# Kernel optimization log

Measured on AMD Instinct MI355X. Metric: run time of the kernel, lower is better.

Reference implementation:

```python
import jax, jax.numpy as jnp
import numpy as np

B, S, D, H, L = 2, 2048, 768, 12, 12
DH = D // H
REL_POS_BINS, MAX_REL_POS = 32, 128
REL_2D_POS_BINS, MAX_REL_2D_POS = 64, 256
LN_EPS = 1e-12


def setup_inputs() -> dict:
    key = jax.random.key(0)
    ks = jax.random.split(key, 12)
    s = 0.02
    return {
        "hidden_states": jax.random.normal(ks[0], (B, S, D), jnp.float32),
        "attention_mask": jnp.zeros((B, 1, 1, S), jnp.bool_),  # True = masked
        "position_ids": jnp.sort(jax.random.randint(ks[1], (B, S), 0, 1024), axis=-1),
        "bbox": jax.random.randint(ks[2], (B, S, 4), 0, 1024),
        # stacked per-layer params (torch Linear applied as x @ W + b)
        "q_w": jax.random.normal(ks[3], (L, D, D), jnp.float32) * s,
        "q_b": jnp.zeros((L, D), jnp.float32),
        "k_w": jax.random.normal(ks[4], (L, D, D), jnp.float32) * s,
        "k_b": jnp.zeros((L, D), jnp.float32),
        "v_w": jax.random.normal(ks[5], (L, D, D), jnp.float32) * s,
        "v_b": jnp.zeros((L, D), jnp.float32),
        "o_w": jax.random.normal(ks[6], (L, D, D), jnp.float32) * s,
        "o_b": jnp.zeros((L, D), jnp.float32),
        "ln_g": jnp.ones((L, D), jnp.float32),
        "ln_b": jnp.zeros((L, D), jnp.float32),
        # rel-pos bias heads x buckets (nn.Linear(bins, heads, bias=False).weight)
        "rel_pos_bias_w": jax.random.normal(ks[7], (H, REL_POS_BINS), jnp.float32) * s,
        "rel_x_bias_w": jax.random.normal(ks[8], (H, REL_2D_POS_BINS), jnp.float32) * s,
        "rel_y_bias_w": jax.random.normal(ks[9], (H, REL_2D_POS_BINS), jnp.float32) * s,
    }


def _rel_bucket(rel, num_buckets, max_distance):
    # bidirectional bucketing from Mesh-TF / ErnieLayout
    nb = num_buckets // 2
    ret = (rel > 0).astype(jnp.int32) * nb
    n = jnp.abs(rel).astype(jnp.int32)
    max_exact = nb // 2
    is_small = n < max_exact
    nf = jnp.maximum(n, 1).astype(jnp.float32)  # avoid log(0); masked by is_small
    val_large = max_exact + (
        jnp.log(nf / max_exact) / np.log(max_distance / max_exact) * (nb - max_exact)
    ).astype(jnp.int32)
    val_large = jnp.minimum(val_large, nb - 1)
    return ret + jnp.where(is_small, n, val_large)


def _bias_from_table(ids_1d, table, num_buckets, max_distance):
    # ids_1d: [B,S] int; table: [H, buckets] -> bias [B,H,S,S]
    rel = ids_1d[:, None, :] - ids_1d[:, :, None]  # memory - query
    buckets = _rel_bucket(rel, num_buckets, max_distance)  # [B,S,S]
    return jnp.transpose(table.T[buckets], (0, 3, 1, 2))  # one-hot @ W.T == gather


def _layer_norm(x, g, b):
    m = jnp.mean(x, axis=-1, keepdims=True)
    v = jnp.mean((x - m) ** 2, axis=-1, keepdims=True)
    return (x - m) / jnp.sqrt(v + LN_EPS) * g + b


def reference(hidden_states, attention_mask, position_ids, bbox,
              q_w, q_b, k_w, k_b, v_w, v_b, o_w, o_b, ln_g, ln_b,
              rel_pos_bias_w, rel_x_bias_w, rel_y_bias_w):
    rel_pos = _bias_from_table(position_ids, rel_pos_bias_w, REL_POS_BINS, MAX_REL_POS)
    rel_2d = (_bias_from_table(bbox[:, :, 0], rel_x_bias_w, REL_2D_POS_BINS, MAX_REL_2D_POS)
              + _bias_from_table(bbox[:, :, 3], rel_y_bias_w, REL_2D_POS_BINS, MAX_REL_2D_POS))
    bias = rel_pos + rel_2d  # [B,H,S,S], shared across layers
    neg = jnp.finfo(jnp.float32).min
    inv_sqrt_dh = 1.0 / np.sqrt(DH)

    def layer(h, p):
        qw, qb, kw, kb, vw, vb, ow, ob, g, bb = p
        q = (h @ qw + qb).reshape(B, S, H, DH).transpose(0, 2, 1, 3) * inv_sqrt_dh
        k = (h @ kw + kb).reshape(B, S, H, DH).transpose(0, 2, 1, 3)
        v = (h @ vw + vb).reshape(B, S, H, DH).transpose(0, 2, 1, 3)
        scores = jnp.einsum('bhqd,bhkd->bhqk', q, k) + bias
        scores = jnp.where(attention_mask, neg, scores)
        probs = jax.nn.softmax(scores, axis=-1)
        ctx = jnp.einsum('bhqk,bhkd->bhqd', probs, v).transpose(0, 2, 1, 3).reshape(B, S, D)
        out = ctx @ ow + ob  # ErnieLayoutSelfOutput dense
        return _layer_norm(out + h, g, bb), None

    h, _ = jax.lax.scan(layer, hidden_states,
                        (q_w, q_b, k_w, k_b, v_w, v_b, o_w, o_b, ln_g, ln_b))
    return h
```

## Files before the change

### kernel.cpp

```cpp
#include <hip/hip_runtime.h>


#define BB 2
#define SS 2048
#define DD 768
#define HH 12
#define NLAYER 12
#define MM 4096

typedef unsigned short u16;
typedef __attribute__((ext_vector_type(8))) short bf16x8;
typedef __attribute__((ext_vector_type(4))) float f32x4;

#define LOG2E 1.44269504088896340736f

__device__ __forceinline__ u16 f2bf(float f) {
  unsigned u = __float_as_uint(f);
  unsigned r = (u + 0x7FFFu + ((u >> 16) & 1u)) >> 16;
  return (u16)r;
}
__device__ __forceinline__ float bf2f(unsigned u) {
  return __uint_as_float(u << 16);
}
__device__ __forceinline__ unsigned cvtpk(float a, float b) {
  unsigned r;
  asm("v_cvt_pk_bf16_f32 %0, %1, %2" : "=v"(r) : "v"(a), "v"(b));
  return r;
}
__device__ __forceinline__ float exp2v(float x) {
  float r;
  asm("v_exp_f32 %0, %1" : "=v"(r) : "v"(x));
  return r;
}

__device__ __forceinline__ void g2lds16(const void* g, void* l) {
  __builtin_amdgcn_global_load_lds(
      (const __attribute__((address_space(1))) unsigned int*)g,
      (__attribute__((address_space(3))) unsigned int*)l, 16, 0, 0);
}

__global__ __launch_bounds__(256) void k_hb(const float4* __restrict__ x,
                                            uint2* __restrict__ o, int n4) {
  int i = blockIdx.x * 256 + threadIdx.x;
  if (i < n4) {
    float4 v = x[i];
    uint2 r;
    r.x = (unsigned)f2bf(v.x) | ((unsigned)f2bf(v.y) << 16);
    r.y = (unsigned)f2bf(v.z) | ((unsigned)f2bf(v.w) << 16);
    o[i] = r;
  }
}

__device__ __forceinline__ int bucket1(int rel) {
  int ret = rel > 0 ? 16 : 0;
  int n = rel < 0 ? -rel : rel;
  if (n < 8) return ret + n;
  int v = 8 + (int)(logf((float)n * 0.125f) * 2.8853900817779268f);
  return ret + (v < 15 ? v : 15);
}
__device__ __forceinline__ int bucket2(int rel) {
  int ret = rel > 0 ? 32 : 0;
  int n = rel < 0 ? -rel : rel;
  if (n < 16) return ret + n;
  int v = 16 + (int)(logf((float)n * 0.0625f) * 5.7707801635558537f);
  return ret + (v < 31 ? v : 31);
}

__global__ __launch_bounds__(256) void k_bias(
    const int* __restrict__ pos, const int* __restrict__ bbx,
    const unsigned char* __restrict__ msk,
    const float* __restrict__ wp, const float* __restrict__ wx,
    const float* __restrict__ wy, u16* __restrict__ bias) {
  int bid = blockIdx.x;
  int b = bid >> 10, qt = (bid >> 5) & 31, kt = bid & 31;
  __shared__ float swp[384], swx[768], swy[768];
  __shared__ int pq[64], xq[64], yq[64], pk[64], xk[64], yk[64];
  __shared__ unsigned char mk[64];
  int t = threadIdx.x;
  for (int i = t; i < 384; i += 256) swp[i] = wp[i];
  for (int i = t; i < 768; i += 256) { swx[i] = wx[i]; swy[i] = wy[i]; }
  int q0 = qt * 64, k0 = kt * 64;
  if (t < 64) {
    int gi = b * SS + q0 + t;
    pq[t] = pos[gi]; xq[t] = bbx[gi * 4]; yq[t] = bbx[gi * 4 + 3];
  } else if (t < 128) {
    int j = t - 64, gi = b * SS + k0 + j;
    pk[j] = pos[gi]; xk[j] = bbx[gi * 4]; yk[j] = bbx[gi * 4 + 3];
    mk[j] = msk[b * SS + k0 + j];
  }
  __syncthreads();
  int w = t >> 6, l = t & 63;
  int hi = l >> 4;
  int qlr = w * 16 + (l & 15);
  int pql = pq[qlr], xql = xq[qlr], yql = yq[qlr];
  int packed[16];
#pragma unroll
  for (int fn = 0; fn < 4; fn++)
#pragma unroll
    for (int r = 0; r < 4; r++) {
      int kl = fn * 16 + hi * 4 + r;
      int b1 = bucket1(pk[kl] - pql);
      int b2 = bucket2(xk[kl] - xql);
      int b3 = bucket2(yk[kl] - yql);
      packed[fn * 4 + r] = b1 | (b2 << 5) | (b3 << 11) | (mk[kl] ? (1 << 17) : 0);
    }
  for (int h = 0; h < 12; h++) {
    const float* rp = swp + h * 32;
    const float* rx = swx + h * 64;
    const float* ry = swy + h * 64;
    unsigned pk2[8];
#pragma unroll
    for (int j = 0; j < 8; j++) {
      int p0 = packed[2 * j], p1 = packed[2 * j + 1];
      float f0 = (rp[p0 & 31] + rx[(p0 >> 5) & 63] + ry[(p0 >> 11) & 63]) * LOG2E;
      float f1 = (rp[p1 & 31] + rx[(p1 >> 5) & 63] + ry[(p1 >> 11) & 63]) * LOG2E;
      if (p0 >> 17) f0 = -3.0e38f;
      if (p1 >> 17) f1 = -3.0e38f;
      pk2[j] = (unsigned)f2bf(f0) | ((unsigned)f2bf(f1) << 16);
    }
    u16* dst = bias +
        ((size_t)((b * 12 + h) * 1024 + qt * 32 + kt) * 256 + t) * 16;
    ((uint4*)dst)[0] = make_uint4(pk2[0], pk2[1], pk2[2], pk2[3]);
    ((uint4*)dst)[1] = make_uint4(pk2[4], pk2[5], pk2[6], pk2[7]);
  }
}

__global__ __launch_bounds__(256) void k_wconv(
    const float* __restrict__ qw, const float* __restrict__ kw,
    const float* __restrict__ vw, const float* __restrict__ ow, int layer,
    u16* __restrict__ wt) {
  int bid = blockIdx.x;
  int g = bid / 576, rr_ = bid % 576, nt = rr_ / 24, kt = rr_ % 24;
  const float* src = g == 0 ? qw : g == 1 ? kw : g == 2 ? vw : ow;
  src += (size_t)layer * DD * DD;
  __shared__ float sm[32][33];
  int t = threadIdx.x, c = t & 31, r0 = t >> 5;
#pragma unroll
  for (int p = 0; p < 4; p++) {
    int rr = r0 + p * 8;
    sm[rr][c] = src[(size_t)(kt * 32 + rr) * DD + nt * 32 + c];
  }
  __syncthreads();
  u16* dst = wt + (size_t)g * DD * DD;
#pragma unroll
  for (int p = 0; p < 4; p++) {
    int rn = r0 + p * 8;
    dst[(size_t)(nt * 32 + rn) * DD + kt * 32 + c] = f2bf(sm[c][rn]);
  }
}

__device__ __forceinline__ void gemm_core(const u16* __restrict__ A,
                                          const u16* __restrict__ Bt, u16* As,
                                          u16* Bs, f32x4 acc[4][4], int tid) {
  int w = tid >> 6, l = tid & 63;
  int wm = w >> 1, wn = w & 1;
#pragma unroll
  for (int i = 0; i < 4; i++)
#pragma unroll
    for (int j = 0; j < 4; j++) acc[i][j] = f32x4{0.f, 0.f, 0.f, 0.f};
  for (int kt = 0; kt < 12; kt++) {
    __syncthreads();
    int r0 = w * 32;
#pragma unroll
    for (int j = 0; j < 4; j++) {
      int row = r0 + j * 8 + (l >> 3);
      int sl = (l & 7) ^ (row & 7);
      g2lds16(A + (size_t)row * DD + kt * 64 + sl * 8, As + (r0 + j * 8) * 64);
      g2lds16(Bt + (size_t)row * DD + kt * 64 + sl * 8, Bs + (r0 + j * 8) * 64);
    }
    __syncthreads();
#pragma unroll
    for (int kk = 0; kk < 2; kk++) {
      bf16x8 af[4], bfr[4];
#pragma unroll
      for (int fm = 0; fm < 4; fm++) {
        int row = wm * 64 + fm * 16 + (l & 15);
        int slot = (kk * 4 + (l >> 4)) ^ (row & 7);
        af[fm] = *(const bf16x8*)((const char*)As + row * 128 + slot * 16);
      }
#pragma unroll
      for (int fn = 0; fn < 4; fn++) {
        int row = wn * 64 + fn * 16 + (l & 15);
        int slot = (kk * 4 + (l >> 4)) ^ (row & 7);
        bfr[fn] = *(const bf16x8*)((const char*)Bs + row * 128 + slot * 16);
      }
#pragma unroll
      for (int fm = 0; fm < 4; fm++)
#pragma unroll
        for (int fn = 0; fn < 4; fn++)
          acc[fm][fn] = __builtin_amdgcn_mfma_f32_16x16x32_bf16(
              af[fm], bfr[fn], acc[fm][fn], 0, 0, 0);
    }
  }
}

__global__ __launch_bounds__(256) void k_gemm_qkv(
    const u16* __restrict__ hb, const u16* __restrict__ wt,
    const float* __restrict__ qbias, const float* __restrict__ kbias,
    const float* __restrict__ vbias, u16* __restrict__ qo, u16* __restrict__ ko,
    u16* __restrict__ vo) {
  __shared__ __align__(16) u16 As[128 * 64];
  __shared__ __align__(16) u16 Bs[128 * 64];
  int bid = blockIdx.x;
  int mblk = bid / 18, nblk = bid % 18;
  int g = nblk / 6, nb = nblk % 6;
  const u16* A = hb + (size_t)mblk * 128 * DD;
  const u16* Bt = wt + (size_t)g * DD * DD + (size_t)nb * 128 * DD;
  f32x4 acc[4][4];
  gemm_core(A, Bt, As, Bs, acc, threadIdx.x);
  const float* bias = g == 0 ? qbias : g == 1 ? kbias : vbias;
  u16* out = g == 0 ? qo : g == 1 ? ko : vo;
  float scale = g == 0 ? 0.125f * LOG2E : 1.0f;
  int w = threadIdx.x >> 6, l = threadIdx.x & 63;
  int wm = w >> 1, wn = w & 1;
#pragma unroll
  for (int fn = 0; fn < 4; fn++) {
    int col = nb * 128 + wn * 64 + fn * 16 + (l & 15);
    float bval = bias[col];
#pragma unroll
    for (int fm = 0; fm < 4; fm++)
#pragma unroll
      for (int r = 0; r < 4; r++) {
        int row = mblk * 128 + wm * 64 + fm * 16 + ((l >> 4) << 2) + r;
        out[(size_t)row * DD + col] = f2bf((acc[fm][fn][r] + bval) * scale);
      }
  }
}

__global__ __launch_bounds__(256) void k_gemm_o(const u16* __restrict__ ctx,
                                                const u16* __restrict__ wto,
                                                const float* __restrict__ obias,
                                                float* __restrict__ outp) {
  __shared__ __align__(16) u16 As[128 * 64];
  __shared__ __align__(16) u16 Bs[128 * 64];
  int bid = blockIdx.x;
  int mblk = bid / 6, nblk = bid % 6;
  const u16* A = ctx + (size_t)mblk * 128 * DD;
  const u16* Bt = wto + (size_t)nblk * 128 * DD;
  f32x4 acc[4][4];
  gemm_core(A, Bt, As, Bs, acc, threadIdx.x);
  int w = threadIdx.x >> 6, l = threadIdx.x & 63;
  int wm = w >> 1, wn = w & 1;
#pragma unroll
  for (int fn = 0; fn < 4; fn++) {
    int col = nblk * 128 + wn * 64 + fn * 16 + (l & 15);
    float bval = obias[col];
#pragma unroll
    for (int fm = 0; fm < 4; fm++)
#pragma unroll
      for (int r = 0; r < 4; r++) {
        int row = mblk * 128 + wm * 64 + fm * 16 + ((l >> 4) << 2) + r;
        outp[(size_t)row * DD + col] = acc[fm][fn][r] + bval;
      }
  }
}

__global__ __launch_bounds__(256) void k_vt(const u16* __restrict__ vo,
                                            u16* __restrict__ vt) {
  int bid = blockIdx.x;
  int bh = bid >> 5, st = bid & 31;
  int b = bh / 12, h = bh % 12;
  int s0 = st * 64;
  __shared__ u16 sm[64][68];
  int t = threadIdx.x, c = t & 63, r0 = t >> 6;
#pragma unroll
  for (int p = 0; p < 16; p++) {
    int r = r0 + p * 4;
    sm[r][c] = vo[(size_t)(b * SS + s0 + r) * DD + h * 64 + c];
  }
  __syncthreads();
#pragma unroll
  for (int p = 0; p < 16; p++) {
    int d = r0 + p * 4;
    vt[(size_t)(bh * 64 + d) * SS + s0 + c] = sm[c][d];
  }
}

__global__ __launch_bounds__(256) void k_attn(
    const u16* __restrict__ qm, const u16* __restrict__ kmat,
    const u16* __restrict__ vt, const u16* __restrict__ bias,
    u16* __restrict__ ctx) {
  int bid = blockIdx.x;
  int qt = bid & 31, bh = bid >> 5;
  int b = bh / 12, h = bh % 12;
  __shared__ __align__(16) u16 Ks[2][64 * 64];
  __shared__ __align__(16) u16 Vs[2][64 * 64];
  __shared__ __align__(16) u16 Ps[4][16 * 64];
  int tid = threadIdx.x, w = tid >> 6, l = tid & 63;
  int hi = l >> 4, qr = l & 15;
  int q0 = qt * 64;
  const u16* qp = qm + (size_t)(b * SS + q0 + w * 16 + qr) * DD + h * 64 +
                  hi * 8;
  bf16x8 aq0 = *(const bf16x8*)qp;
  bf16x8 aq1 = *(const bf16x8*)(qp + 32);
  const u16* kb_ = kmat + (size_t)(b * SS) * DD + h * 64;
  const u16* vb_ = vt + (size_t)bh * 64 * SS;
  const u16* bb_ = bias + ((size_t)(bh * 32 + qt) * 32 * 256 + tid) * 16;
  f32x4 oa[4];
#pragma unroll
  for (int fn = 0; fn < 4; fn++) oa[fn] = f32x4{0.f, 0.f, 0.f, 0.f};
  float m_ = -3.0e38f, l_ = 0.f;
  int srow = tid >> 3, sc8 = tid & 7;

  auto STAGE = [&](int kt, int buf) {
#pragma unroll
    for (int j = 0; j < 2; j++) {
      int rr = srow + j * 32;
      int sl = sc8 ^ (rr & 7);
      g2lds16(kb_ + (size_t)(kt * 64 + rr) * DD + sl * 8,
              &Ks[buf][tid * 8 + j * 2048]);
      g2lds16(vb_ + (size_t)rr * SS + kt * 64 + sl * 8,
              &Vs[buf][tid * 8 + j * 2048]);
    }
  };

  STAGE(0, 0);
  uint4 bu0 = ((const uint4*)bb_)[0];
  uint4 bu1 = ((const uint4*)bb_)[1];
  uint4 nb0 = bu0, nb1 = bu1;
  char* pw = (char*)&Ps[w][0] + qr * 128;
  int qs = (qr & 7) << 4;
  __syncthreads();

  for (int kt = 0; kt < 32; kt++) {
    int buf = kt & 1;
    if (kt < 31) STAGE(kt + 1, buf ^ 1);
    f32x4 sc[4];
#pragma unroll
    for (int fn = 0; fn < 4; fn++) sc[fn] = f32x4{0.f, 0.f, 0.f, 0.f};
#pragma unroll
    for (int kk = 0; kk < 2; kk++) {
      bf16x8 aq = kk == 0 ? aq0 : aq1;
#pragma unroll
      for (int fn = 0; fn < 4; fn++) {
        int row = fn * 16 + qr;
        int slot = (kk * 4 + hi) ^ (row & 7);
        bf16x8 bk = *(const bf16x8*)((const char*)&Ks[buf][0] + row * 128 +
                                     slot * 16);
        sc[fn] = __builtin_amdgcn_mfma_f32_16x16x32_bf16(bk, aq, sc[fn],
                                                         0, 0, 0);
      }
    }
    unsigned ua[8] = {bu0.x, bu0.y, bu0.z, bu0.w, bu1.x, bu1.y, bu1.z, bu1.w};
#pragma unroll
    for (int fn = 0; fn < 4; fn++)
#pragma unroll
      for (int r = 0; r < 4; r++) {
        int i = fn * 4 + r;
        unsigned uv = ua[i >> 1];
        sc[fn][r] += bf2f((i & 1) ? (uv >> 16) : (uv & 0xffffu));
      }
    if (kt < 31) {
      const uint4* bpn = (const uint4*)(bb_ + (size_t)(kt + 1) * 4096);
      nb0 = bpn[0];
      nb1 = bpn[1];
    }
    float pm = fmaxf(fmaxf(fmaxf(sc[0][0], sc[0][1]), fmaxf(sc[0][2], sc[0][3])),
                     fmaxf(fmaxf(sc[1][0], sc[1][1]), fmaxf(sc[1][2], sc[1][3])));
    pm = fmaxf(pm,
         fmaxf(fmaxf(fmaxf(sc[2][0], sc[2][1]), fmaxf(sc[2][2], sc[2][3])),
               fmaxf(fmaxf(sc[3][0], sc[3][1]), fmaxf(sc[3][2], sc[3][3]))));
    pm = fmaxf(pm, __shfl_xor(pm, 16));
    pm = fmaxf(pm, __shfl_xor(pm, 32));
    if (__any(pm > m_)) {
      float mn = fmaxf(m_, pm);
      float f = exp2v(m_ - mn);
#pragma unroll
      for (int fn = 0; fn < 4; fn++)
#pragma unroll
        for (int r = 0; r < 4; r++) oa[fn][r] *= f;
      l_ *= f;
      m_ = mn;
    }
    float rs = 0.f;
#pragma unroll
    for (int fn = 0; fn < 4; fn++)
#pragma unroll
      for (int r = 0; r < 4; r++) {
        float pv = exp2v(sc[fn][r] - m_);
        sc[fn][r] = pv;
        rs += pv;
      }
    rs += __shfl_xor(rs, 16);
    rs += __shfl_xor(rs, 32);
    l_ += rs;
#pragma unroll
    for (int fn = 0; fn < 4; fn++) {
      unsigned w0 = cvtpk(sc[fn][0], sc[fn][1]);
      unsigned w1 = cvtpk(sc[fn][2], sc[fn][3]);
      *(uint2*)(pw + ((fn * 32 + hi * 8) ^ qs)) = make_uint2(w0, w1);
    }
#pragma unroll
    for (int ck = 0; ck < 2; ck++) {
      bf16x8 pt = *(const bf16x8*)(pw + ((ck * 64 + hi * 16) ^ qs));
#pragma unroll
      for (int fn = 0; fn < 4; fn++) {
        int row = fn * 16 + qr;
        int slot = (ck * 4 + hi) ^ (row & 7);
        bf16x8 av = *(const bf16x8*)((const char*)&Vs[buf][0] + row * 128 +
                                     slot * 16);
        oa[fn] = __builtin_amdgcn_mfma_f32_16x16x32_bf16(av, pt, oa[fn],
                                                         0, 0, 0);
      }
    }
    bu0 = nb0;
    bu1 = nb1;
    __syncthreads();
  }
  float inv = 1.0f / l_;
  u16* cp = ctx + (size_t)(b * SS + q0 + w * 16 + qr) * DD + h * 64 + hi * 4;
#pragma unroll
  for (int fn = 0; fn < 4; fn++) {
    unsigned w0 = cvtpk(oa[fn][0] * inv, oa[fn][1] * inv);
    unsigned w1 = cvtpk(oa[fn][2] * inv, oa[fn][3] * inv);
    *(uint2*)(cp + fn * 16) = make_uint2(w0, w1);
  }
}

__global__ __launch_bounds__(256) void k_ln(const float* __restrict__ x,
                                            const float* __restrict__ res,
                                            const float* __restrict__ g,
                                            const float* __restrict__ bta,
                                            float* __restrict__ ho,
                                            u16* __restrict__ hbo) {
  int row = blockIdx.x;
  int t = threadIdx.x;
  const float* xr = x + (size_t)row * DD;
  const float* rr = res + (size_t)row * DD;
  float v[3];
  float s = 0.f, s2 = 0.f;
#pragma unroll
  for (int j = 0; j < 3; j++) {
    float a = xr[t + j * 256] + rr[t + j * 256];
    v[j] = a;
    s += a;
    s2 += a * a;
  }
#pragma unroll
  for (int m = 1; m < 64; m <<= 1) {
    s += __shfl_xor(s, m);
    s2 += __shfl_xor(s2, m);
  }
  __shared__ float red[8];
  int w = t >> 6, l = t & 63;
  if (l == 0) { red[w] = s; red[4 + w] = s2; }
  __syncthreads();
  s = red[0] + red[1] + red[2] + red[3];
  s2 = red[4] + red[5] + red[6] + red[7];
  float mean = s * (1.f / 768.f);
  float var = s2 * (1.f / 768.f) - mean * mean;
  float rstd = rsqrtf(var + 1e-12f);
#pragma unroll
  for (int j = 0; j < 3; j++) {
    int c = t + j * 256;
    float y = (v[j] - mean) * rstd * g[c] + bta[c];
    ho[(size_t)row * DD + c] = y;
    hbo[(size_t)row * DD + c] = f2bf(y);
  }
}

extern "C" void kernel_launch(void* const* d_in, const int* in_sizes, int n_in,
                              void* d_out, int out_size, void* d_ws,
                              size_t ws_size, hipStream_t stream) {
  const float* hid = (const float*)d_in[0];
  const unsigned char* msk = (const unsigned char*)d_in[1];
  const int* pos = (const int*)d_in[2];
  const int* bbx = (const int*)d_in[3];
  const float* qw = (const float*)d_in[4];
  const float* qbv = (const float*)d_in[5];
  const float* kw = (const float*)d_in[6];
  const float* kbv = (const float*)d_in[7];
  const float* vw = (const float*)d_in[8];
  const float* vbv = (const float*)d_in[9];
  const float* ow = (const float*)d_in[10];
  const float* obv = (const float*)d_in[11];
  const float* lng = (const float*)d_in[12];
  const float* lnb = (const float*)d_in[13];
  const float* wpb = (const float*)d_in[14];
  const float* wxb = (const float*)d_in[15];
  const float* wyb = (const float*)d_in[16];
  float* outp = (float*)d_out;

  char* p = (char*)d_ws;
  u16* bias = (u16*)p;   p += (size_t)201326592;
  float* hbuf = (float*)p; p += 12582912;
  u16* hb = (u16*)p;     p += 6291456;
  u16* qo = (u16*)p;     p += 6291456;
  u16* ko = (u16*)p;     p += 6291456;
  u16* vo = (u16*)p;     p += 6291456;
  u16* vtb = (u16*)p;    p += 6291456;
  u16* ctxb = (u16*)p;   p += 6291456;
  u16* wtb = (u16*)p;    p += 4718592;
  float* att = (float*)qo;

  k_hb<<<dim3(3072), dim3(256), 0, stream>>>((const float4*)hid, (uint2*)hb,
                                             786432);
  k_bias<<<dim3(2048), dim3(256), 0, stream>>>(pos, bbx, msk, wpb, wxb, wyb,
                                               bias);
  for (int l = 0; l < NLAYER; l++) {
    k_wconv<<<dim3(2304), dim3(256), 0, stream>>>(qw, kw, vw, ow, l, wtb);
    k_gemm_qkv<<<dim3(576), dim3(256), 0, stream>>>(
        hb, wtb, qbv + l * DD, kbv + l * DD, vbv + l * DD, qo, ko, vo);
    k_vt<<<dim3(768), dim3(256), 0, stream>>>(vo, vtb);
    k_attn<<<dim3(768), dim3(256), 0, stream>>>(qo, ko, vtb, bias, ctxb);
    k_gemm_o<<<dim3(192), dim3(256), 0, stream>>>(
        ctxb, wtb + (size_t)3 * DD * DD, obv + l * DD, att);
    k_ln<<<dim3(4096), dim3(256), 0, stream>>>(
        att, l == 0 ? hid : (const float*)hbuf, lng + l * DD, lnb + l * DD,
        l == 11 ? outp : hbuf, hb);
  }
}
```

Baseline: 1.622 ms.

## Triple-buffer attention, MFMA row sums, lazy rescale, and retile bias/wconv/LN kernels

Attention moves to a three-stage K/V ring with one barrier per step and explicit vmcnt waits, and issues the next bias load earlier. The bias now seeds the score accumulator, row sums come from an extra MFMA against a ones vector, and max rescaling is skipped unless the max grows by more than 8 in log2 units. The bias kernel now handles 4 heads per block with float4 table lookups. The weight transpose uses 64x64 tiles with packed stores, and layer norm uses one wavefront per row with no shared-memory reduction. The lazy rescale lets exponentials reach up to 2^8 before renormalising, which can cost some accuracy and risks overflow in bf16.

```diff
diff --git a/kernel.cpp b/kernel.cpp
--- a/kernel.cpp
+++ b/kernel.cpp
@@ -72,13 +72,15 @@
     const float* __restrict__ wp, const float* __restrict__ wx,
     const float* __restrict__ wy, u16* __restrict__ bias) {
   int bid = blockIdx.x;
-  int b = bid >> 10, qt = (bid >> 5) & 31, kt = bid & 31;
-  __shared__ float swp[384], swx[768], swy[768];
+  int g = bid >> 11, rem = bid & 2047;
+  int b = rem >> 10, qt = (rem >> 5) & 31, kt = rem & 31;
+  __shared__ __align__(16) float swpT[32][4], swxT[64][4], swyT[64][4];
   __shared__ int pq[64], xq[64], yq[64], pk[64], xk[64], yk[64];
   __shared__ unsigned char mk[64];
   int t = threadIdx.x;
-  for (int i = t; i < 384; i += 256) swp[i] = wp[i];
-  for (int i = t; i < 768; i += 256) { swx[i] = wx[i]; swy[i] = wy[i]; }
+  if (t < 128) swpT[t >> 2][t & 3] = wp[(g * 4 + (t & 3)) * 32 + (t >> 2)];
+  { int i = t; swxT[i >> 2][i & 3] = wx[(g * 4 + (i & 3)) * 64 + (i >> 2)];
+    swyT[i >> 2][i & 3] = wy[(g * 4 + (i & 3)) * 64 + (i >> 2)]; }
   int q0 = qt * 64, k0 = kt * 64;
   if (t < 64) {
     int gi = b * SS + q0 + t;
@@ -104,24 +106,40 @@
       int b3 = bucket2(yk[kl] - yql);
       packed[fn * 4 + r] = b1 | (b2 << 5) | (b3 << 11) | (mk[kl] ? (1 << 17) : 0);
     }
-  for (int h = 0; h < 12; h++) {
-    const float* rp = swp + h * 32;
-    const float* rx = swx + h * 64;
-    const float* ry = swy + h * 64;
-    unsigned pk2[8];
-#pragma unroll
-    for (int j = 0; j < 8; j++) {
-      int p0 = packed[2 * j], p1 = packed[2 * j + 1];
-      float f0 = (rp[p0 & 31] + rx[(p0 >> 5) & 63] + ry[(p0 >> 11) & 63]) * LOG2E;
-      float f1 = (rp[p1 & 31] + rx[(p1 >> 5) & 63] + ry[(p1 >> 11) & 63]) * LOG2E;
-      if (p0 >> 17) f0 = -3.0e38f;
-      if (p1 >> 17) f1 = -3.0e38f;
-      pk2[j] = (unsigned)f2bf(f0) | ((unsigned)f2bf(f1) << 16);
-    }
+  unsigned pk2[4][8];
+#pragma unroll
+  for (int j2 = 0; j2 < 8; j2++) {
+    float a0[4], a1[4];
+    {
+      int p = packed[2 * j2];
+      f32x4 ap = *(const f32x4*)swpT[p & 31];
+      f32x4 bx = *(const f32x4*)swxT[(p >> 5) & 63];
+      f32x4 cy = *(const f32x4*)swyT[(p >> 11) & 63];
+      bool mm = (p >> 17) != 0;
+#pragma unroll
+      for (int hh = 0; hh < 4; hh++)
+        a0[hh] = mm ? -3.0e38f : (ap[hh] + bx[hh] + cy[hh]) * LOG2E;
+    }
+    {
+      int p = packed[2 * j2 + 1];
+      f32x4 ap = *(const f32x4*)swpT[p & 31];
+      f32x4 bx = *(const f32x4*)swxT[(p >> 5) & 63];
+      f32x4 cy = *(const f32x4*)swyT[(p >> 11) & 63];
+      bool mm = (p >> 17) != 0;
+#pragma unroll
+      for (int hh = 0; hh < 4; hh++)
+        a1[hh] = mm ? -3.0e38f : (ap[hh] + bx[hh] + cy[hh]) * LOG2E;
+    }
+#pragma unroll
+    for (int hh = 0; hh < 4; hh++) pk2[hh][j2] = cvtpk(a0[hh], a1[hh]);
+  }
+#pragma unroll
+  for (int hh = 0; hh < 4; hh++) {
+    int h = g * 4 + hh;
     u16* dst = bias +
         ((size_t)((b * 12 + h) * 1024 + qt * 32 + kt) * 256 + t) * 16;
-    ((uint4*)dst)[0] = make_uint4(pk2[0], pk2[1], pk2[2], pk2[3]);
-    ((uint4*)dst)[1] = make_uint4(pk2[4], pk2[5], pk2[6], pk2[7]);
+    ((uint4*)dst)[0] = make_uint4(pk2[hh][0], pk2[hh][1], pk2[hh][2], pk2[hh][3]);
+    ((uint4*)dst)[1] = make_uint4(pk2[hh][4], pk2[hh][5], pk2[hh][6], pk2[hh][7]);
   }
 }
 
@@ -130,22 +148,25 @@
     const float* __restrict__ vw, const float* __restrict__ ow, int layer,
     u16* __restrict__ wt) {
   int bid = blockIdx.x;
-  int g = bid / 576, rr_ = bid % 576, nt = rr_ / 24, kt = rr_ % 24;
+  int g = bid / 144, rr_ = bid % 144, nt = rr_ / 12, kt = rr_ % 12;
   const float* src = g == 0 ? qw : g == 1 ? kw : g == 2 ? vw : ow;
   src += (size_t)layer * DD * DD;
-  __shared__ float sm[32][33];
-  int t = threadIdx.x, c = t & 31, r0 = t >> 5;
-#pragma unroll
-  for (int p = 0; p < 4; p++) {
-    int rr = r0 + p * 8;
-    sm[rr][c] = src[(size_t)(kt * 32 + rr) * DD + nt * 32 + c];
+  __shared__ float sm[64][67];
+  int t = threadIdx.x, c2 = t & 31, r0 = t >> 5;
+#pragma unroll
+  for (int p = 0; p < 8; p++) {
+    int row = r0 + p * 8;
+    float2 v = *(const float2*)&src[(size_t)(kt * 64 + row) * DD + nt * 64 + c2 * 2];
+    sm[row][c2 * 2] = v.x;
+    sm[row][c2 * 2 + 1] = v.y;
   }
   __syncthreads();
   u16* dst = wt + (size_t)g * DD * DD;
 #pragma unroll
-  for (int p = 0; p < 4; p++) {
-    int rn = r0 + p * 8;
-    dst[(size_t)(nt * 32 + rn) * DD + kt * 32 + c] = f2bf(sm[c][rn]);
+  for (int p = 0; p < 8; p++) {
+    int n = r0 + p * 8;
+    float v0 = sm[c2 * 2][n], v1 = sm[c2 * 2 + 1][n];
+    *(unsigned*)&dst[(size_t)(nt * 64 + n) * DD + kt * 64 + c2 * 2] = cvtpk(v0, v1);
   }
 }
 
@@ -283,8 +304,8 @@
   int bid = blockIdx.x;
   int qt = bid & 31, bh = bid >> 5;
   int b = bh / 12, h = bh % 12;
-  __shared__ __align__(16) u16 Ks[2][64 * 64];
-  __shared__ __align__(16) u16 Vs[2][64 * 64];
+  __shared__ __align__(16) u16 Ks[3][64 * 64];
+  __shared__ __align__(16) u16 Vs[3][64 * 64];
   __shared__ __align__(16) u16 Ps[4][16 * 64];
   int tid = threadIdx.x, w = tid >> 6, l = tid & 63;
   int hi = l >> 4, qr = l & 15;
@@ -299,7 +320,11 @@
   f32x4 oa[4];
 #pragma unroll
   for (int fn = 0; fn < 4; fn++) oa[fn] = f32x4{0.f, 0.f, 0.f, 0.f};
-  float m_ = -3.0e38f, l_ = 0.f;
+  f32x4 lacc = f32x4{0.f, 0.f, 0.f, 0.f};
+  float m_ = -3.0e38f;
+  bf16x8 vones;
+#pragma unroll
+  for (int i = 0; i < 8; i++) vones[i] = (short)0x3F80;
   int srow = tid >> 3, sc8 = tid & 7;
 
   auto STAGE = [&](int kt, int buf) {
@@ -320,14 +345,30 @@
   uint4 nb0 = bu0, nb1 = bu1;
   char* pw = (char*)&Ps[w][0] + qr * 128;
   int qs = (qr & 7) << 4;
-  __syncthreads();
+  int cur = 0, nxt = 1;
 
   for (int kt = 0; kt < 32; kt++) {
-    int buf = kt & 1;
-    if (kt < 31) STAGE(kt + 1, buf ^ 1);
+    if (kt < 31) {
+      STAGE(kt + 1, nxt);
+      const uint4* bpn = (const uint4*)(bb_ + (size_t)(kt + 1) * 4096);
+      nb0 = bpn[0];
+      nb1 = bpn[1];
+      asm volatile("s_waitcnt vmcnt(6)" ::: "memory");
+    } else {
+      asm volatile("s_waitcnt vmcnt(0)" ::: "memory");
+    }
+    __builtin_amdgcn_s_barrier();
+    __builtin_amdgcn_sched_barrier(0);
+    unsigned ua[8] = {bu0.x, bu0.y, bu0.z, bu0.w, bu1.x, bu1.y, bu1.z, bu1.w};
     f32x4 sc[4];
 #pragma unroll
-    for (int fn = 0; fn < 4; fn++) sc[fn] = f32x4{0.f, 0.f, 0.f, 0.f};
+    for (int fn = 0; fn < 4; fn++)
+#pragma unroll
+      for (int r = 0; r < 4; r++) {
+        int i = fn * 4 + r;
+        unsigned uv = ua[i >> 1];
+        sc[fn][r] = bf2f((i & 1) ? (uv >> 16) : (uv & 0xffffu));
+      }
 #pragma unroll
     for (int kk = 0; kk < 2; kk++) {
       bf16x8 aq = kk == 0 ? aq0 : aq1;
@@ -335,25 +376,11 @@
       for (int fn = 0; fn < 4; fn++) {
         int row = fn * 16 + qr;
         int slot = (kk * 4 + hi) ^ (row & 7);
-        bf16x8 bk = *(const bf16x8*)((const char*)&Ks[buf][0] + row * 128 +
+        bf16x8 bk = *(const bf16x8*)((const char*)&Ks[cur][0] + row * 128 +
                                      slot * 16);
         sc[fn] = __builtin_amdgcn_mfma_f32_16x16x32_bf16(bk, aq, sc[fn],
                                                          0, 0, 0);
       }
-    }
-    unsigned ua[8] = {bu0.x, bu0.y, bu0.z, bu0.w, bu1.x, bu1.y, bu1.z, bu1.w};
-#pragma unroll
-    for (int fn = 0; fn < 4; fn++)
-#pragma unroll
-      for (int r = 0; r < 4; r++) {
-        int i = fn * 4 + r;
-        unsigned uv = ua[i >> 1];
-        sc[fn][r] += bf2f((i & 1) ? (uv >> 16) : (uv & 0xffffu));
-      }
-    if (kt < 31) {
-      const uint4* bpn = (const uint4*)(bb_ + (size_t)(kt + 1) * 4096);
-      nb0 = bpn[0];
-      nb1 = bpn[1];
     }
     float pm = fmaxf(fmaxf(fmaxf(sc[0][0], sc[0][1]), fmaxf(sc[0][2], sc[0][3])),
                      fmaxf(fmaxf(sc[1][0], sc[1][1]), fmaxf(sc[1][2], sc[1][3])));
@@ -362,28 +389,21 @@
                fmaxf(fmaxf(sc[3][0], sc[3][1]), fmaxf(sc[3][2], sc[3][3]))));
     pm = fmaxf(pm, __shfl_xor(pm, 16));
     pm = fmaxf(pm, __shfl_xor(pm, 32));
-    if (__any(pm > m_)) {
+    if (__any(pm > m_ + 8.f)) {
       float mn = fmaxf(m_, pm);
       float f = exp2v(m_ - mn);
 #pragma unroll
       for (int fn = 0; fn < 4; fn++)
 #pragma unroll
         for (int r = 0; r < 4; r++) oa[fn][r] *= f;
-      l_ *= f;
+#pragma unroll
+      for (int r = 0; r < 4; r++) lacc[r] *= f;
       m_ = mn;
     }
-    float rs = 0.f;
 #pragma unroll
     for (int fn = 0; fn < 4; fn++)
 #pragma unroll
-      for (int r = 0; r < 4; r++) {
-        float pv = exp2v(sc[fn][r] - m_);
-        sc[fn][r] = pv;
-        rs += pv;
-      }
-    rs += __shfl_xor(rs, 16);
-    rs += __shfl_xor(rs, 32);
-    l_ += rs;
+      for (int r = 0; r < 4; r++) sc[fn][r] = exp2v(sc[fn][r] - m_);
 #pragma unroll
     for (int fn = 0; fn < 4; fn++) {
       unsigned w0 = cvtpk(sc[fn][0], sc[fn][1]);
@@ -397,17 +417,19 @@
       for (int fn = 0; fn < 4; fn++) {
         int row = fn * 16 + qr;
         int slot = (ck * 4 + hi) ^ (row & 7);
-        bf16x8 av = *(const bf16x8*)((const char*)&Vs[buf][0] + row * 128 +
+        bf16x8 av = *(const bf16x8*)((const char*)&Vs[cur][0] + row * 128 +
                                      slot * 16);
         oa[fn] = __builtin_amdgcn_mfma_f32_16x16x32_bf16(av, pt, oa[fn],
                                                          0, 0, 0);
       }
+      lacc = __builtin_amdgcn_mfma_f32_16x16x32_bf16(vones, pt, lacc, 0, 0, 0);
     }
     bu0 = nb0;
     bu1 = nb1;
-    __syncthreads();
-  }
-  float inv = 1.0f / l_;
+    cur = nxt;
+    nxt = nxt + 1 == 3 ? 0 : nxt + 1;
+  }
+  float inv = 1.0f / lacc[0];
   u16* cp = ctx + (size_t)(b * SS + q0 + w * 16 + qr) * DD + h * 64 + hi * 4;
 #pragma unroll
   for (int fn = 0; fn < 4; fn++) {
@@ -423,15 +445,15 @@
                                             const float* __restrict__ bta,
                                             float* __restrict__ ho,
                                             u16* __restrict__ hbo) {
-  int row = blockIdx.x;
-  int t = threadIdx.x;
+  int w = threadIdx.x >> 6, l = threadIdx.x & 63;
+  int row = blockIdx.x * 4 + w;
   const float* xr = x + (size_t)row * DD;
   const float* rr = res + (size_t)row * DD;
-  float v[3];
+  float v[12];
   float s = 0.f, s2 = 0.f;
 #pragma unroll
-  for (int j = 0; j < 3; j++) {
-    float a = xr[t + j * 256] + rr[t + j * 256];
+  for (int j = 0; j < 12; j++) {
+    float a = xr[l + j * 64] + rr[l + j * 64];
     v[j] = a;
     s += a;
     s2 += a * a;
@@ -441,18 +463,12 @@
     s += __shfl_xor(s, m);
     s2 += __shfl_xor(s2, m);
   }
-  __shared__ float red[8];
-  int w = t >> 6, l = t & 63;
-  if (l == 0) { red[w] = s; red[4 + w] = s2; }
-  __syncthreads();
-  s = red[0] + red[1] + red[2] + red[3];
-  s2 = red[4] + red[5] + red[6] + red[7];
   float mean = s * (1.f / 768.f);
   float var = s2 * (1.f / 768.f) - mean * mean;
   float rstd = rsqrtf(var + 1e-12f);
 #pragma unroll
-  for (int j = 0; j < 3; j++) {
-    int c = t + j * 256;
+  for (int j = 0; j < 12; j++) {
+    int c = l + j * 64;
     float y = (v[j] - mean) * rstd * g[c] + bta[c];
     ho[(size_t)row * DD + c] = y;
     hbo[(size_t)row * DD + c] = f2bf(y);
@@ -495,17 +511,17 @@
 
   k_hb<<<dim3(3072), dim3(256), 0, stream>>>((const float4*)hid, (uint2*)hb,
                                              786432);
-  k_bias<<<dim3(2048), dim3(256), 0, stream>>>(pos, bbx, msk, wpb, wxb, wyb,
+  k_bias<<<dim3(6144), dim3(256), 0, stream>>>(pos, bbx, msk, wpb, wxb, wyb,
                                                bias);
   for (int l = 0; l < NLAYER; l++) {
-    k_wconv<<<dim3(2304), dim3(256), 0, stream>>>(qw, kw, vw, ow, l, wtb);
+    k_wconv<<<dim3(576), dim3(256), 0, stream>>>(qw, kw, vw, ow, l, wtb);
     k_gemm_qkv<<<dim3(576), dim3(256), 0, stream>>>(
         hb, wtb, qbv + l * DD, kbv + l * DD, vbv + l * DD, qo, ko, vo);
     k_vt<<<dim3(768), dim3(256), 0, stream>>>(vo, vtb);
     k_attn<<<dim3(768), dim3(256), 0, stream>>>(qo, ko, vtb, bias, ctxb);
     k_gemm_o<<<dim3(192), dim3(256), 0, stream>>>(
         ctxb, wtb + (size_t)3 * DD * DD, obv + l * DD, att);
-    k_ln<<<dim3(4096), dim3(256), 0, stream>>>(
+    k_ln<<<dim3(1024), dim3(256), 0, stream>>>(
         att, l == 0 ? hid : (const float*)hbuf, lng + l * DD, lnb + l * DD,
         l == 11 ? outp : hbuf, hb);
   }
```

New measurement: 1.831 ms. 1.13x slower.
